# Performance work log

Hardware: AMD Instinct MI355X
Metric: run time of the kernel (lower is better)

Reference implementation:

```python
import jax, jax.numpy as jnp
import numpy as np
import math

N_HEADS = 8
EMBED = 128
HEAD_DEPTH = EMBED // N_HEADS
CLIP = 10.0
NEG_INF = 1.0e10
SCALE = math.sqrt(HEAD_DEPTH)


def setup_inputs() -> dict:
    key = jax.random.key(0)
    ks = jax.random.split(key, 8)
    B, C, N = 32, 2, 512
    Q = jax.random.normal(ks[0], (B, C, N, EMBED), dtype=jnp.float32)
    K = jax.random.normal(ks[1], (B, C, N, EMBED), dtype=jnp.float32)
    V = jax.random.normal(ks[2], (B, C, N, EMBED), dtype=jnp.float32)
    mask = jax.random.bernoulli(ks[3], 0.15, (B, C, N, 1))  # True = masked out
    stdv_qkv = 1.0 / math.sqrt(HEAD_DEPTH)
    stdv_out = 1.0 / math.sqrt(EMBED)
    # torch nn.Linear weights: (out_features, in_features)
    Wq = jax.random.uniform(ks[4], (EMBED, EMBED), jnp.float32, -stdv_qkv, stdv_qkv)
    Wk = jax.random.uniform(ks[5], (EMBED, EMBED), jnp.float32, -stdv_qkv, stdv_qkv)
    Wv = jax.random.uniform(ks[6], (EMBED, EMBED), jnp.float32, -stdv_qkv, stdv_qkv)
    Wout = jax.random.uniform(ks[7], (EMBED, EMBED), jnp.float32, -stdv_out, stdv_out)
    return {"Q": Q, "K": K, "V": V, "mask": mask,
            "Wq": Wq, "Wk": Wk, "Wv": Wv, "Wout": Wout}


def _split_heads(T):
    # (b, c, n, E) -> (b, H, c, n, d)
    b, c, n, _ = T.shape
    return T.reshape(b, c, n, N_HEADS, HEAD_DEPTH).transpose(0, 3, 1, 2, 4)


def reference(Q, K, V, mask, Wq, Wk, Wv, Wout):
    # Linear projections (torch Linear: y = x @ W.T)
    q = _split_heads(jnp.einsum('bcne,fe->bcnf', Q, Wq))
    k = _split_heads(jnp.einsum('bcne,fe->bcnf', K, Wk))
    v = _split_heads(jnp.einsum('bcne,fe->bcnf', V, Wv))
    # logits: (b, H, c, q, k)
    logits = jnp.einsum('bhcqd,bhckd->bhcqk', q, k) / SCALE
    logits = CLIP * jnp.tanh(logits)
    # mask (b, c, n, 1) -> (b, 1, c, 1, n); True -> -1e10
    m = mask[:, None, :, :, :].swapaxes(-1, -2)
    logits = jnp.where(m, -NEG_INF, logits)
    probs = jax.nn.softmax(logits, axis=-1)
    out = jnp.einsum('bhcqk,bhckd->bhcqd', probs, v)
    # combine heads: (b, H, c, n, d) -> (b, c, n, E)
    b, h, c, n, d = out.shape
    out = out.transpose(0, 2, 3, 1, 4).reshape(b, c, n, EMBED)
    return jnp.einsum('bcne,fe->bcnf', out, Wout)
```

## Files before the change

kernel.cpp:

```cpp
#include <hip/hip_runtime.h>

typedef _Float16 half_t;
typedef _Float16 half8 __attribute__((ext_vector_type(8)));
typedef _Float16 half4 __attribute__((ext_vector_type(4)));
typedef float floatx4 __attribute__((ext_vector_type(4)));
typedef float floatx16 __attribute__((ext_vector_type(16)));

#define C1 0.72134752044448170368f
#define C2 14.4269504088896340736f
#define C3 28.8539008177792681472f

__device__ __forceinline__ floatx4 zero4() {
    floatx4 z; z[0] = z[1] = z[2] = z[3] = 0.f; return z;
}
__device__ __forceinline__ floatx16 zero16() {
    floatx16 z;
#pragma unroll
    for (int i = 0; i < 16; ++i) z[i] = 0.f;
    return z;
}

__device__ __forceinline__ float pfun(float sp, float b) {
    float u = __builtin_amdgcn_exp2f(sp);
    float r = __builtin_amdgcn_rcpf(u + 1.0f);
    return __builtin_amdgcn_exp2f(b - C3 * r);
}

__global__ void k_convw(const float* __restrict__ Wq, const float* __restrict__ Wk,
                        const float* __restrict__ Wv, const float* __restrict__ Wo,
                        half_t* __restrict__ Wh) {
    int idx = blockIdx.x * 256 + threadIdx.x;
    int which = idx >> 14;
    int off = idx & 16383;
    const float* src = (which == 0) ? Wq : (which == 1) ? Wk : (which == 2) ? Wv : Wo;
    float scale = (which == 0) ? C1 : 1.0f;
    Wh[idx] = (half_t)(src[off] * scale);
}

__global__ __launch_bounds__(256) void k_proj(
        const float* __restrict__ Q, const float* __restrict__ K,
        const float* __restrict__ V, const half_t* __restrict__ WhBase,
        half_t* __restrict__ qw, half_t* __restrict__ kw, half_t* __restrict__ vw) {
    int which = blockIdx.y;
    const float* X = (which == 0) ? Q : (which == 1) ? K : V;
    const half_t* W = WhBase + which * 16384;
    half_t* Y = (which == 0) ? qw : (which == 1) ? kw : vw;

    int tid = threadIdx.x;
    int w = tid >> 6, lane = tid & 63;
    int l15 = lane & 15, quad = lane >> 4;
    int rowbase = blockIdx.x * 64 + w * 16;
    int arow = rowbase + l15;

    floatx4 acc[8];
#pragma unroll
    for (int nt = 0; nt < 8; ++nt) acc[nt] = zero4();

#pragma unroll
    for (int ks = 0; ks < 4; ++ks) {
        const float* ap = X + arow * 128 + ks * 32 + quad * 8;
        float4 a0 = *(const float4*)ap;
        float4 a1 = *(const float4*)(ap + 4);
        half8 af;
        af[0] = (half_t)a0.x; af[1] = (half_t)a0.y; af[2] = (half_t)a0.z; af[3] = (half_t)a0.w;
        af[4] = (half_t)a1.x; af[5] = (half_t)a1.y; af[6] = (half_t)a1.z; af[7] = (half_t)a1.w;
#pragma unroll
        for (int nt = 0; nt < 8; ++nt) {
            half8 bf = *(const half8*)(W + (nt * 16 + l15) * 128 + ks * 32 + quad * 8);
            acc[nt] = __builtin_amdgcn_mfma_f32_16x16x32_f16(af, bf, acc[nt], 0, 0, 0);
        }
    }
#pragma unroll
    for (int nt = 0; nt < 8; ++nt) {
#pragma unroll
        for (int r = 0; r < 4; ++r) {
            int R = rowbase + quad * 4 + r;
            int bc = R >> 9, n = R & 511;
            Y[((bc * 8 + nt) * 512 + n) * 16 + l15] = (half_t)acc[nt][r];
        }
    }
}

__global__ __launch_bounds__(256, 2) void k_attn(
        const half_t* __restrict__ qg, const half_t* __restrict__ kg,
        const half_t* __restrict__ vg, const int* __restrict__ mask,
        half_t* __restrict__ attn) {
    __shared__ float bias[512];
    __shared__ half_t vT[16 * 520];
    __shared__ half_t Pl[4][128 * 44];

    int bch = blockIdx.x;
    int bc = bch >> 3, h = bch & 7;
    int tid = threadIdx.x;
    int w = tid >> 6, lane = tid & 63;
    int l31 = lane & 31, hf = lane >> 5;
    int l15 = lane & 15, quad = lane >> 4;

    const half_t* qh = qg + bch * 8192;
    const half_t* kh = kg + bch * 8192;
    const half_t* vh = vg + bch * 8192;

    for (int i = tid; i < 512; i += 256)
        bias[i] = mask[bc * 512 + i] ? -1.0e30f : C2;
    for (int r = tid; r < 512; r += 256) {
        half8 v0 = *(const half8*)(vh + r * 16);
        half8 v1 = *(const half8*)(vh + r * 16 + 8);
#pragma unroll
        for (int d = 0; d < 8; ++d) vT[d * 520 + r] = v0[d];
#pragma unroll
        for (int d = 0; d < 8; ++d) vT[(d + 8) * 520 + r] = v1[d];
    }
    __syncthreads();

    half8 qf[4];
#pragma unroll
    for (int t = 0; t < 4; ++t)
        qf[t] = *(const half8*)(qh + ((w * 4 + t) * 32 + l31) * 16 + hf * 8);

    floatx4 O[8];
#pragma unroll
    for (int nt = 0; nt < 8; ++nt) O[nt] = zero4();
    float rs[4] = {0.f, 0.f, 0.f, 0.f};
    half_t* Pw = &Pl[w][0];

#pragma unroll 1
    for (int c = 0; c < 16; ++c) {
        half8 kf = *(const half8*)(kh + (c * 32 + l31) * 16 + hf * 8);
        half8 vf = *(const half8*)(&vT[l15 * 520 + c * 32 + quad * 8]);
        const float4* b4 = (const float4*)bias;
        float4 bv[4];
#pragma unroll
        for (int g = 0; g < 4; ++g) bv[g] = b4[c * 8 + hf + 2 * g];

#pragma unroll
        for (int t = 0; t < 4; ++t) {
            floatx16 S = __builtin_amdgcn_mfma_f32_32x32x16_f16(kf, qf[t], zero16(), 0, 0, 0);
            int prow = (t * 32 + l31) * 44;
            float rsum = 0.f;
#pragma unroll
            for (int g = 0; g < 4; ++g) {
                float p0 = pfun(S[4 * g + 0], bv[g].x);
                float p1 = pfun(S[4 * g + 1], bv[g].y);
                float p2 = pfun(S[4 * g + 2], bv[g].z);
                float p3 = pfun(S[4 * g + 3], bv[g].w);
                rsum += (p0 + p1) + (p2 + p3);
                half4 ph;
                ph[0] = (half_t)p0; ph[1] = (half_t)p1;
                ph[2] = (half_t)p2; ph[3] = (half_t)p3;
                *(half4*)(Pw + prow + hf * 4 + g * 8) = ph;
            }
            rs[t] += rsum;
        }
#pragma unroll
        for (int nt = 0; nt < 8; ++nt) {
            half8 pb = *(const half8*)(Pw + (nt * 16 + l15) * 44 + quad * 8);
            O[nt] = __builtin_amdgcn_mfma_f32_16x16x32_f16(vf, pb, O[nt], 0, 0, 0);
        }
    }

    float inv[4];
#pragma unroll
    for (int t = 0; t < 4; ++t) {
        float r2 = rs[t] + __shfl_xor(rs[t], 32, 64);
        inv[t] = __builtin_amdgcn_rcpf(r2);
    }
#pragma unroll
    for (int nt = 0; nt < 8; ++nt) {
        float iv = __shfl(inv[nt >> 1], ((nt & 1) << 4) | l15, 64);
        int qrow = w * 128 + nt * 16 + l15;
        half4 ov;
        ov[0] = (half_t)(O[nt][0] * iv);
        ov[1] = (half_t)(O[nt][1] * iv);
        ov[2] = (half_t)(O[nt][2] * iv);
        ov[3] = (half_t)(O[nt][3] * iv);
        *(half4*)(attn + (bc * 512 + qrow) * 128 + h * 16 + quad * 4) = ov;
    }
}

__global__ __launch_bounds__(256) void k_out(
        const half_t* __restrict__ A, const half_t* __restrict__ Wh,
        float* __restrict__ out) {
    int tid = threadIdx.x;
    int w = tid >> 6, lane = tid & 63;
    int l15 = lane & 15, quad = lane >> 4;
    int rowbase = blockIdx.x * 64 + w * 16;

    floatx4 acc[8];
#pragma unroll
    for (int nt = 0; nt < 8; ++nt) acc[nt] = zero4();
#pragma unroll
    for (int ks = 0; ks < 4; ++ks) {
        half8 af = *(const half8*)(A + (rowbase + l15) * 128 + ks * 32 + quad * 8);
#pragma unroll
        for (int nt = 0; nt < 8; ++nt) {
            half8 bf = *(const half8*)(Wh + (nt * 16 + l15) * 128 + ks * 32 + quad * 8);
            acc[nt] = __builtin_amdgcn_mfma_f32_16x16x32_f16(af, bf, acc[nt], 0, 0, 0);
        }
    }
#pragma unroll
    for (int nt = 0; nt < 8; ++nt)
#pragma unroll
        for (int r = 0; r < 4; ++r)
            out[(rowbase + quad * 4 + r) * 128 + nt * 16 + l15] = acc[nt][r];
}

extern "C" void kernel_launch(void* const* d_in, const int* in_sizes, int n_in,
                              void* d_out, int out_size, void* d_ws, size_t ws_size,
                              hipStream_t stream) {
    const float* Q    = (const float*)d_in[0];
    const float* K    = (const float*)d_in[1];
    const float* V    = (const float*)d_in[2];
    const int*   mask = (const int*)d_in[3];
    const float* Wq   = (const float*)d_in[4];
    const float* Wk   = (const float*)d_in[5];
    const float* Wv   = (const float*)d_in[6];
    const float* Wo   = (const float*)d_in[7];
    float* out = (float*)d_out;

    half_t* ws = (half_t*)d_ws;
    half_t* Wh = ws;
    half_t* qw = ws + 65536;
    half_t* kw = qw + 4194304;
    half_t* vw = kw + 4194304;
    half_t* aw = vw + 4194304;

    k_convw<<<256, 256, 0, stream>>>(Wq, Wk, Wv, Wo, Wh);
    k_proj<<<dim3(512, 3), 256, 0, stream>>>(Q, K, V, Wh, qw, kw, vw);
    k_attn<<<512, 256, 0, stream>>>(qw, kw, vw, mask, aw);
    k_out<<<512, 256, 0, stream>>>(aw, Wh + 49152, out);
}
```

Measured before the change: 192.4 us.

## Write V pre-transposed from projection, split attention blocks over query halves

```diff
diff --git a/kernel.cpp b/kernel.cpp
--- a/kernel.cpp
+++ b/kernel.cpp
@@ -44,13 +44,11 @@
     int which = blockIdx.y;
     const float* X = (which == 0) ? Q : (which == 1) ? K : V;
     const half_t* W = WhBase + which * 16384;
-    half_t* Y = (which == 0) ? qw : (which == 1) ? kw : vw;
 
     int tid = threadIdx.x;
     int w = tid >> 6, lane = tid & 63;
     int l15 = lane & 15, quad = lane >> 4;
-    int rowbase = blockIdx.x * 64 + w * 16;
-    int arow = rowbase + l15;
+    int tokbase = blockIdx.x * 64 + w * 16;
 
     floatx4 acc[8];
 #pragma unroll
@@ -58,38 +56,60 @@
 
 #pragma unroll
     for (int ks = 0; ks < 4; ++ks) {
-        const float* ap = X + arow * 128 + ks * 32 + quad * 8;
+        const float* ap = X + (tokbase + l15) * 128 + ks * 32 + quad * 8;
         float4 a0 = *(const float4*)ap;
         float4 a1 = *(const float4*)(ap + 4);
-        half8 af;
-        af[0] = (half_t)a0.x; af[1] = (half_t)a0.y; af[2] = (half_t)a0.z; af[3] = (half_t)a0.w;
-        af[4] = (half_t)a1.x; af[5] = (half_t)a1.y; af[6] = (half_t)a1.z; af[7] = (half_t)a1.w;
+        half8 xf;
+        xf[0] = (half_t)a0.x; xf[1] = (half_t)a0.y; xf[2] = (half_t)a0.z; xf[3] = (half_t)a0.w;
+        xf[4] = (half_t)a1.x; xf[5] = (half_t)a1.y; xf[6] = (half_t)a1.z; xf[7] = (half_t)a1.w;
+        if (which == 2) {
+#pragma unroll
+            for (int nt = 0; nt < 8; ++nt) {
+                half8 wf = *(const half8*)(W + (nt * 16 + l15) * 128 + ks * 32 + quad * 8);
+                acc[nt] = __builtin_amdgcn_mfma_f32_16x16x32_f16(xf, wf, acc[nt], 0, 0, 0);
+            }
+        } else {
+#pragma unroll
+            for (int nt = 0; nt < 8; ++nt) {
+                half8 wf = *(const half8*)(W + (nt * 16 + l15) * 128 + ks * 32 + quad * 8);
+                acc[nt] = __builtin_amdgcn_mfma_f32_16x16x32_f16(wf, xf, acc[nt], 0, 0, 0);
+            }
+        }
+    }
+
+    if (which == 2) {
+        int R0 = tokbase + quad * 4;
+        int bc = R0 >> 9, n0 = R0 & 511;
 #pragma unroll
         for (int nt = 0; nt < 8; ++nt) {
-            half8 bf = *(const half8*)(W + (nt * 16 + l15) * 128 + ks * 32 + quad * 8);
-            acc[nt] = __builtin_amdgcn_mfma_f32_16x16x32_f16(af, bf, acc[nt], 0, 0, 0);
-        }
-    }
-#pragma unroll
-    for (int nt = 0; nt < 8; ++nt) {
-#pragma unroll
-        for (int r = 0; r < 4; ++r) {
-            int R = rowbase + quad * 4 + r;
-            int bc = R >> 9, n = R & 511;
-            Y[((bc * 8 + nt) * 512 + n) * 16 + l15] = (half_t)acc[nt][r];
-        }
-    }
-}
-
-__global__ __launch_bounds__(256, 2) void k_attn(
+            half4 hv;
+            hv[0] = (half_t)acc[nt][0]; hv[1] = (half_t)acc[nt][1];
+            hv[2] = (half_t)acc[nt][2]; hv[3] = (half_t)acc[nt][3];
+            *(half4*)(vw + ((bc * 8 + nt) * 16 + l15) * 512 + n0) = hv;
+        }
+    } else {
+        int R = tokbase + l15;
+        int bc = R >> 9, n = R & 511;
+        half_t* Y = (which == 0) ? qw : kw;
+#pragma unroll
+        for (int nt = 0; nt < 8; ++nt) {
+            half4 hv;
+            hv[0] = (half_t)acc[nt][0]; hv[1] = (half_t)acc[nt][1];
+            hv[2] = (half_t)acc[nt][2]; hv[3] = (half_t)acc[nt][3];
+            *(half4*)(Y + ((bc * 8 + nt) * 512 + n) * 16 + quad * 4) = hv;
+        }
+    }
+}
+
+__global__ __launch_bounds__(256, 4) void k_attn(
         const half_t* __restrict__ qg, const half_t* __restrict__ kg,
-        const half_t* __restrict__ vg, const int* __restrict__ mask,
+        const half_t* __restrict__ vTg, const int* __restrict__ mask,
         half_t* __restrict__ attn) {
     __shared__ float bias[512];
-    __shared__ half_t vT[16 * 520];
-    __shared__ half_t Pl[4][128 * 44];
-
-    int bch = blockIdx.x;
+    __shared__ half_t Pl[4][32 * 36];
+
+    int bx = blockIdx.x;
+    int bch = bx >> 1, qhi = bx & 1;
     int bc = bch >> 3, h = bch & 7;
     int tid = threadIdx.x;
     int w = tid >> 6, lane = tid & 63;
@@ -98,44 +118,36 @@
 
     const half_t* qh = qg + bch * 8192;
     const half_t* kh = kg + bch * 8192;
-    const half_t* vh = vg + bch * 8192;
+    const half_t* vh = vTg + bch * 8192;
 
     for (int i = tid; i < 512; i += 256)
         bias[i] = mask[bc * 512 + i] ? -1.0e30f : C2;
-    for (int r = tid; r < 512; r += 256) {
-        half8 v0 = *(const half8*)(vh + r * 16);
-        half8 v1 = *(const half8*)(vh + r * 16 + 8);
-#pragma unroll
-        for (int d = 0; d < 8; ++d) vT[d * 520 + r] = v0[d];
-#pragma unroll
-        for (int d = 0; d < 8; ++d) vT[(d + 8) * 520 + r] = v1[d];
-    }
     __syncthreads();
 
-    half8 qf[4];
-#pragma unroll
-    for (int t = 0; t < 4; ++t)
-        qf[t] = *(const half8*)(qh + ((w * 4 + t) * 32 + l31) * 16 + hf * 8);
-
-    floatx4 O[8];
-#pragma unroll
-    for (int nt = 0; nt < 8; ++nt) O[nt] = zero4();
-    float rs[4] = {0.f, 0.f, 0.f, 0.f};
+    int qbase = qhi * 256 + w * 64;
+    half8 qf[2];
+#pragma unroll
+    for (int t = 0; t < 2; ++t)
+        qf[t] = *(const half8*)(qh + (qbase + t * 32 + l31) * 16 + hf * 8);
+
+    floatx4 O[4];
+#pragma unroll
+    for (int nt = 0; nt < 4; ++nt) O[nt] = zero4();
+    float rs[2] = {0.f, 0.f};
     half_t* Pw = &Pl[w][0];
+    const float4* b4 = (const float4*)bias;
 
 #pragma unroll 1
     for (int c = 0; c < 16; ++c) {
         half8 kf = *(const half8*)(kh + (c * 32 + l31) * 16 + hf * 8);
-        half8 vf = *(const half8*)(&vT[l15 * 520 + c * 32 + quad * 8]);
-        const float4* b4 = (const float4*)bias;
+        half8 vf = *(const half8*)(vh + l15 * 512 + c * 32 + quad * 8);
         float4 bv[4];
 #pragma unroll
         for (int g = 0; g < 4; ++g) bv[g] = b4[c * 8 + hf + 2 * g];
 
 #pragma unroll
-        for (int t = 0; t < 4; ++t) {
+        for (int t = 0; t < 2; ++t) {
             floatx16 S = __builtin_amdgcn_mfma_f32_32x32x16_f16(kf, qf[t], zero16(), 0, 0, 0);
-            int prow = (t * 32 + l31) * 44;
             float rsum = 0.f;
 #pragma unroll
             for (int g = 0; g < 4; ++g) {
@@ -147,27 +159,27 @@
                 half4 ph;
                 ph[0] = (half_t)p0; ph[1] = (half_t)p1;
                 ph[2] = (half_t)p2; ph[3] = (half_t)p3;
-                *(half4*)(Pw + prow + hf * 4 + g * 8) = ph;
+                *(half4*)(Pw + l31 * 36 + hf * 4 + g * 8) = ph;
             }
             rs[t] += rsum;
-        }
-#pragma unroll
-        for (int nt = 0; nt < 8; ++nt) {
-            half8 pb = *(const half8*)(Pw + (nt * 16 + l15) * 44 + quad * 8);
-            O[nt] = __builtin_amdgcn_mfma_f32_16x16x32_f16(vf, pb, O[nt], 0, 0, 0);
-        }
-    }
-
-    float inv[4];
-#pragma unroll
-    for (int t = 0; t < 4; ++t) {
+#pragma unroll
+            for (int nt2 = 0; nt2 < 2; ++nt2) {
+                half8 pb = *(const half8*)(Pw + (nt2 * 16 + l15) * 36 + quad * 8);
+                O[2 * t + nt2] = __builtin_amdgcn_mfma_f32_16x16x32_f16(vf, pb, O[2 * t + nt2], 0, 0, 0);
+            }
+        }
+    }
+
+    float inv[2];
+#pragma unroll
+    for (int t = 0; t < 2; ++t) {
         float r2 = rs[t] + __shfl_xor(rs[t], 32, 64);
         inv[t] = __builtin_amdgcn_rcpf(r2);
     }
 #pragma unroll
-    for (int nt = 0; nt < 8; ++nt) {
+    for (int nt = 0; nt < 4; ++nt) {
         float iv = __shfl(inv[nt >> 1], ((nt & 1) << 4) | l15, 64);
-        int qrow = w * 128 + nt * 16 + l15;
+        int qrow = qbase + nt * 16 + l15;
         half4 ov;
         ov[0] = (half_t)(O[nt][0] * iv);
         ov[1] = (half_t)(O[nt][1] * iv);
@@ -183,25 +195,26 @@
     int tid = threadIdx.x;
     int w = tid >> 6, lane = tid & 63;
     int l15 = lane & 15, quad = lane >> 4;
-    int rowbase = blockIdx.x * 64 + w * 16;
+    int tokbase = blockIdx.x * 64 + w * 16;
 
     floatx4 acc[8];
 #pragma unroll
     for (int nt = 0; nt < 8; ++nt) acc[nt] = zero4();
 #pragma unroll
     for (int ks = 0; ks < 4; ++ks) {
-        half8 af = *(const half8*)(A + (rowbase + l15) * 128 + ks * 32 + quad * 8);
+        half8 xf = *(const half8*)(A + (tokbase + l15) * 128 + ks * 32 + quad * 8);
 #pragma unroll
         for (int nt = 0; nt < 8; ++nt) {
-            half8 bf = *(const half8*)(Wh + (nt * 16 + l15) * 128 + ks * 32 + quad * 8);
-            acc[nt] = __builtin_amdgcn_mfma_f32_16x16x32_f16(af, bf, acc[nt], 0, 0, 0);
-        }
-    }
-#pragma unroll
-    for (int nt = 0; nt < 8; ++nt)
-#pragma unroll
-        for (int r = 0; r < 4; ++r)
-            out[(rowbase + quad * 4 + r) * 128 + nt * 16 + l15] = acc[nt][r];
+            half8 wf = *(const half8*)(Wh + (nt * 16 + l15) * 128 + ks * 32 + quad * 8);
+            acc[nt] = __builtin_amdgcn_mfma_f32_16x16x32_f16(wf, xf, acc[nt], 0, 0, 0);
+        }
+    }
+#pragma unroll
+    for (int nt = 0; nt < 8; ++nt) {
+        float4 o;
+        o.x = acc[nt][0]; o.y = acc[nt][1]; o.z = acc[nt][2]; o.w = acc[nt][3];
+        *(float4*)(out + (tokbase + l15) * 128 + nt * 16 + quad * 4) = o;
+    }
 }
 
 extern "C" void kernel_launch(void* const* d_in, const int* in_sizes, int n_in,
@@ -226,6 +239,6 @@
 
     k_convw<<<256, 256, 0, stream>>>(Wq, Wk, Wv, Wo, Wh);
     k_proj<<<dim3(512, 3), 256, 0, stream>>>(Q, K, V, Wh, qw, kw, vw);
-    k_attn<<<512, 256, 0, stream>>>(qw, kw, vw, mask, aw);
+    k_attn<<<1024, 256, 0, stream>>>(qw, kw, vw, mask, aw);
     k_out<<<512, 256, 0, stream>>>(aw, Wh + 49152, out);
 }
```

Result: faster. 188.2 us (-2.2%).
